# Performance work log

Hardware: AMD Instinct MI355X
Metric: run time of the kernel (lower is better)

The kernel has to match this reference:

```python
import jax, jax.numpy as jnp
import numpy as np

N_GRAPHS = 256
N_NODES = 100000
N_EDGES = 1000000
EMB = 64
EMB_RBF = 16
NUM_HEADS = 1


def setup_inputs() -> dict:
    key = jax.random.key(0)
    ks = jax.random.split(key, 10)
    edge_emb = jax.random.normal(ks[0], (N_EDGES, EMB), dtype=jnp.float32)
    edge_index = jax.random.randint(ks[1], (2, N_EDGES), 0, N_NODES, dtype=jnp.int64)
    distance_vec = jax.random.normal(ks[2], (N_EDGES, 3), dtype=jnp.float32)
    lattice = jax.random.normal(ks[3], (N_GRAPHS, 3, 3), dtype=jnp.float32)
    batch = jnp.sort(jax.random.randint(ks[4], (N_NODES,), 0, N_GRAPHS, dtype=jnp.int64))
    rbf = jax.random.uniform(ks[5], (N_EDGES, EMB_RBF), dtype=jnp.float32)
    # Dense layers (GemNet Dense defaults to bias=False)
    s = 1.0 / np.sqrt(EMB)
    W1 = jax.random.normal(ks[6], (EMB, EMB), dtype=jnp.float32) * s
    W2 = jax.random.normal(ks[7], (EMB, EMB), dtype=jnp.float32) * s
    W_rbf = jax.random.normal(ks[8], (EMB_RBF, EMB), dtype=jnp.float32) * (1.0 / np.sqrt(EMB_RBF))
    W_out = jax.random.normal(ks[9], (EMB, NUM_HEADS), dtype=jnp.float32) * s
    return {"edge_emb": edge_emb, "edge_index": edge_index, "distance_vec": distance_vec,
            "lattice": lattice, "batch": batch, "rbf": rbf,
            "W1": W1, "W2": W2, "W_rbf": W_rbf, "W_out": W_out}


def reference(edge_emb, edge_index, distance_vec, lattice, batch, rbf, W1, W2, W_rbf, W_out):
    # compute_score_per_edge: MLP on edge embeddings, gated by RBF projection
    h = jax.nn.silu(edge_emb @ W1)            # [E, EMB]
    x_F = h @ W2                               # [E, EMB]
    x_F = x_F * (rbf @ W_rbf)                  # RBF gate, [E, EMB]
    edge_scores = x_F @ W_out                  # [E, num_heads]

    batch_edge = batch[edge_index[0]]          # graph id per edge, [E]
    # normalize_score=True: divide by edge count per graph
    num_edges = jax.ops.segment_sum(jnp.ones((edge_scores.shape[0],), dtype=edge_scores.dtype),
                                    batch_edge, num_segments=N_GRAPHS)
    edge_scores = edge_scores / num_edges[batch_edge, None]

    # edge_score_to_lattice_score_frac_symmetric, summed over heads (num_heads=1)
    s = edge_scores[:, 0]                      # [E]
    unit = distance_vec / jnp.linalg.norm(distance_vec, axis=-1, keepdims=True)
    outer = s[:, None, None] * unit[:, :, None] * distance_vec[:, None, :]  # [E,3,3]
    sym = 0.5 * (outer + jnp.swapaxes(outer, 1, 2))
    out = jax.ops.segment_sum(sym, batch_edge, num_segments=N_GRAPHS)       # [B,3,3]
    return out
```

## Files before the change

### kernel.cpp

```cpp
#include <hip/hip_runtime.h>
#include <math.h>

constexpr int G    = 256;
constexpr int EMB  = 64;
constexpr int ERBF = 16;

typedef __attribute__((ext_vector_type(8))) short bf16x8;
typedef __attribute__((ext_vector_type(4))) float f32x4;

static __device__ __forceinline__ short bf16_rne(float f) {
    union { float f; unsigned u; } v; v.f = f;
    unsigned r = (v.u + 0x7FFFu + ((v.u >> 16) & 1u)) >> 16;
    return (short)r;
}

__global__ void prep_M_kernel(const float* __restrict__ W2,
                              const float* __restrict__ W_rbf,
                              const float* __restrict__ W_out,
                              float* __restrict__ M) {
    int t = blockIdx.x * blockDim.x + threadIdx.x;
    if (t >= EMB * ERBF) return;
    int p = t >> 4;
    int k = t & 15;
    float acc = 0.f;
    for (int j = 0; j < EMB; ++j)
        acc = fmaf(W2[p * EMB + j] * W_out[j], W_rbf[k * EMB + j], acc);
    M[p * ERBF + k] = acc;
}

__global__ __launch_bounds__(256, 4) void edge_kernel(
    const float* __restrict__ edge_emb,
    const int*   __restrict__ edge_src,
    const float* __restrict__ dvec,
    const int*   __restrict__ batch,
    const float* __restrict__ rbf,
    const float* __restrict__ W1,
    const float* __restrict__ M,
    float* __restrict__ partial,
    int ne, int nblk)
{
    __shared__ float accs[G * 9];

    const int tid  = threadIdx.x;
    const int w    = tid >> 6;
    const int lane = tid & 63;
    const int q    = lane >> 4;
    const int col  = lane & 15;

    for (int i = tid; i < G * 9; i += 256) accs[i] = 0.f;

    bf16x8 w1f[4][2];
#pragma unroll
    for (int nt = 0; nt < 4; ++nt)
#pragma unroll
        for (int c = 0; c < 2; ++c) {
            bf16x8 wv;
#pragma unroll
            for (int j = 0; j < 8; ++j)
                wv[j] = bf16_rne(W1[(c * 32 + q * 8 + j) * EMB + nt * 16 + col]);
            w1f[nt][c] = wv;
        }
    bf16x8 mtf[4];
#pragma unroll
    for (int nt = 0; nt < 4; ++nt) {
        bf16x8 mv;
#pragma unroll
        for (int j = 0; j < 8; ++j) {
            int k = q * 8 + j;
            mv[j] = (k < ERBF) ? bf16_rne(M[(nt * 16 + col) * ERBF + k]) : (short)0;
        }
        mtf[nt] = mv;
    }
    __syncthreads();

    const long estep = (long)nblk * 4 * 16;
    for (long e0 = ((long)blockIdx.x * 4 + w) * 16; e0 < ne; e0 += estep) {
        const long erow  = e0 + col;
        const bool rowok = (erow < ne);

        bf16x8 af[2];
#pragma unroll
        for (int c = 0; c < 2; ++c) {
            bf16x8 a;
            if (rowok) {
                const float4* p = (const float4*)(edge_emb + (size_t)erow * EMB + c * 32 + q * 8);
                float4 v0 = p[0], v1 = p[1];
                a[0] = bf16_rne(v0.x); a[1] = bf16_rne(v0.y);
                a[2] = bf16_rne(v0.z); a[3] = bf16_rne(v0.w);
                a[4] = bf16_rne(v1.x); a[5] = bf16_rne(v1.y);
                a[6] = bf16_rne(v1.z); a[7] = bf16_rne(v1.w);
            } else {
#pragma unroll
                for (int j = 0; j < 8; ++j) a[j] = 0;
            }
            af[c] = a;
        }
        bf16x8 rf;
        if (q < 2 && rowok) {
            const float4* p = (const float4*)(rbf + (size_t)erow * ERBF + q * 8);
            float4 v0 = p[0], v1 = p[1];
            rf[0] = bf16_rne(v0.x); rf[1] = bf16_rne(v0.y);
            rf[2] = bf16_rne(v0.z); rf[3] = bf16_rne(v0.w);
            rf[4] = bf16_rne(v1.x); rf[5] = bf16_rne(v1.y);
            rf[6] = bf16_rne(v1.z); rf[7] = bf16_rne(v1.w);
        } else {
#pragma unroll
            for (int j = 0; j < 8; ++j) rf[j] = 0;
        }

        f32x4 hacc[4], vacc[4];
#pragma unroll
        for (int nt = 0; nt < 4; ++nt) {
            f32x4 z = {0.f, 0.f, 0.f, 0.f};
            z = __builtin_amdgcn_mfma_f32_16x16x32_bf16(af[0], w1f[nt][0], z, 0, 0, 0);
            z = __builtin_amdgcn_mfma_f32_16x16x32_bf16(af[1], w1f[nt][1], z, 0, 0, 0);
            hacc[nt] = z;
            f32x4 zv = {0.f, 0.f, 0.f, 0.f};
            vacc[nt] = __builtin_amdgcn_mfma_f32_16x16x32_bf16(rf, mtf[nt], zv, 0, 0, 0);
        }

        float sc[4];
#pragma unroll
        for (int r = 0; r < 4; ++r) {
            float acc = 0.f;
#pragma unroll
            for (int nt = 0; nt < 4; ++nt) {
                float x = hacc[nt][r];
                float s = x * __builtin_amdgcn_rcpf(1.f + __expf(-x));
                acc = fmaf(s, vacc[nt][r], acc);
            }
            sc[r] = acc;
        }
#pragma unroll
        for (int m = 1; m < 16; m <<= 1) {
#pragma unroll
            for (int r = 0; r < 4; ++r) sc[r] += __shfl_xor(sc[r], m);
        }

        if (col < 4) {
            long e = e0 + q * 4 + col;
            if (e < ne) {
                float s = sc[col];
                int   g = batch[edge_src[e]];
                size_t de = (size_t)e * 3;
                float dx = dvec[de], dy = dvec[de + 1], dz = dvec[de + 2];
                float nrm = sqrtf(dx * dx + dy * dy + dz * dz);
                float cc = s / nrm;
                float* a = &accs[g * 9];
                atomicAdd(a + 0, cc * dx * dx);
                atomicAdd(a + 1, cc * dx * dy);
                atomicAdd(a + 2, cc * dx * dz);
                atomicAdd(a + 3, cc * dy * dy);
                atomicAdd(a + 4, cc * dy * dz);
                atomicAdd(a + 5, cc * dz * dz);
                atomicAdd(a + 6, 1.0f);
            }
        }
    }

    __syncthreads();
    float* outp = partial + (size_t)blockIdx.x * (G * 8);
    {
        int g = tid;
        float* a = &accs[g * 9];
        float4 p0 = {a[0], a[1], a[2], a[3]};
        float4 p1 = {a[4], a[5], a[6], 0.f};
        ((float4*)(outp + g * 8))[0] = p0;
        ((float4*)(outp + g * 8))[1] = p1;
    }
}

__global__ __launch_bounds__(256) void reduce_kernel(
    const float* __restrict__ partial, float* __restrict__ out, int nblk)
{
    int g = blockIdx.x;
    __shared__ float red[256][8];
    float loc[8];
#pragma unroll
    for (int c = 0; c < 8; ++c) loc[c] = 0.f;

    for (int b = threadIdx.x; b < nblk; b += 256) {
        const float4* p = (const float4*)(partial + (size_t)b * (G * 8) + g * 8);
        float4 v0 = p[0], v1 = p[1];
        loc[0] += v0.x; loc[1] += v0.y; loc[2] += v0.z; loc[3] += v0.w;
        loc[4] += v1.x; loc[5] += v1.y; loc[6] += v1.z; loc[7] += v1.w;
    }
#pragma unroll
    for (int c = 0; c < 8; ++c) red[threadIdx.x][c] = loc[c];
    __syncthreads();

    for (int off = 128; off >= 1; off >>= 1) {
        if (threadIdx.x < off) {
#pragma unroll
            for (int c = 0; c < 8; ++c)
                red[threadIdx.x][c] += red[threadIdx.x + off][c];
        }
        __syncthreads();
    }

    if (threadIdx.x == 0) {
        float cnt = red[0][6];
        float inv = (cnt > 0.f) ? (1.f / cnt) : 0.f;
        float xx = red[0][0] * inv, xy = red[0][1] * inv, xz = red[0][2] * inv;
        float yy = red[0][3] * inv, yz = red[0][4] * inv, zz = red[0][5] * inv;
        float* o = out + g * 9;
        o[0] = xx; o[1] = xy; o[2] = xz;
        o[3] = xy; o[4] = yy; o[5] = yz;
        o[6] = xz; o[7] = yz; o[8] = zz;
    }
}

extern "C" void kernel_launch(void* const* d_in, const int* in_sizes, int n_in,
                              void* d_out, int out_size, void* d_ws, size_t ws_size,
                              hipStream_t stream) {
    const float* edge_emb   = (const float*)d_in[0];
    const int*   edge_index = (const int*)  d_in[1];
    const float* dvec       = (const float*)d_in[2];
    const int*   batch      = (const int*)  d_in[4];
    const float* rbf        = (const float*)d_in[5];
    const float* W1         = (const float*)d_in[6];
    const float* W2         = (const float*)d_in[7];
    const float* W_rbf      = (const float*)d_in[8];
    const float* W_out      = (const float*)d_in[9];
    float* out = (float*)d_out;

    int ne = in_sizes[0] / EMB;

    float* M = (float*)d_ws;
    float* partial = (float*)((char*)d_ws + 4096);
    size_t avail = (ws_size > 4096) ? (ws_size - 4096) : 0;
    int nblk = (int)(avail / (G * 8 * sizeof(float)));
    int tiles = (ne + 63) / 64;
    if (nblk > 1024)  nblk = 1024;
    if (nblk > tiles) nblk = tiles;
    if (nblk < 1)     nblk = 1;

    prep_M_kernel<<<4, 256, 0, stream>>>(W2, W_rbf, W_out, M);
    edge_kernel<<<nblk, 256, 0, stream>>>(edge_emb, edge_index, dvec, batch,
                                          rbf, W1, M, partial, ne, nblk);
    reduce_kernel<<<G, 256, 0, stream>>>(partial, out, nblk);
}
```

Measured before the change: 426.9 us.

## Fuse M precompute into edge kernel, hoist gathers, transpose partial layout

Removes the separate prep_M kernel launch: each block recomputes the fused W2·W_out·W_rbf matrix into shared memory. The main loop issues the edge_src, dvec and batch gathers at the top of each iteration, before the MFMA work, and clamps out-of-range rows instead of branching, so the global loads overlap the math. The partial-sum buffer is transposed to be graph-major so the reduce kernel reads contiguously. The grid is capped at 768 blocks with launch bounds of 3 waves per SIMD. The cost is redundant per-block M computation and an extra barrier.

Result: no change. 432.8 us (+1.4%).

```diff
diff --git a/kernel.cpp b/kernel.cpp
--- a/kernel.cpp
+++ b/kernel.cpp
@@ -14,32 +14,21 @@
     return (short)r;
 }
 
-__global__ void prep_M_kernel(const float* __restrict__ W2,
-                              const float* __restrict__ W_rbf,
-                              const float* __restrict__ W_out,
-                              float* __restrict__ M) {
-    int t = blockIdx.x * blockDim.x + threadIdx.x;
-    if (t >= EMB * ERBF) return;
-    int p = t >> 4;
-    int k = t & 15;
-    float acc = 0.f;
-    for (int j = 0; j < EMB; ++j)
-        acc = fmaf(W2[p * EMB + j] * W_out[j], W_rbf[k * EMB + j], acc);
-    M[p * ERBF + k] = acc;
-}
-
-__global__ __launch_bounds__(256, 4) void edge_kernel(
+__global__ __launch_bounds__(256, 3) void edge_kernel(
     const float* __restrict__ edge_emb,
     const int*   __restrict__ edge_src,
     const float* __restrict__ dvec,
     const int*   __restrict__ batch,
     const float* __restrict__ rbf,
     const float* __restrict__ W1,
-    const float* __restrict__ M,
+    const float* __restrict__ W2,
+    const float* __restrict__ W_rbf,
+    const float* __restrict__ W_out,
     float* __restrict__ partial,
     int ne, int nblk)
 {
     __shared__ float accs[G * 9];
+    __shared__ float Msh[EMB * ERBF];
 
     const int tid  = threadIdx.x;
     const int w    = tid >> 6;
@@ -49,6 +38,23 @@
 
     for (int i = tid; i < G * 9; i += 256) accs[i] = 0.f;
 
+    {
+        int idx0 = tid * 4;
+        int p  = idx0 >> 4;
+        int k0 = idx0 & 15;
+        float m0 = 0.f, m1 = 0.f, m2 = 0.f, m3 = 0.f;
+        for (int j = 0; j < EMB; ++j) {
+            float wj = W2[p * EMB + j] * W_out[j];
+            m0 = fmaf(wj, W_rbf[(k0 + 0) * EMB + j], m0);
+            m1 = fmaf(wj, W_rbf[(k0 + 1) * EMB + j], m1);
+            m2 = fmaf(wj, W_rbf[(k0 + 2) * EMB + j], m2);
+            m3 = fmaf(wj, W_rbf[(k0 + 3) * EMB + j], m3);
+        }
+        Msh[idx0 + 0] = m0; Msh[idx0 + 1] = m1;
+        Msh[idx0 + 2] = m2; Msh[idx0 + 3] = m3;
+    }
+    __syncthreads();
+
     bf16x8 w1f[4][2];
 #pragma unroll
     for (int nt = 0; nt < 4; ++nt)
@@ -67,53 +73,63 @@
 #pragma unroll
         for (int j = 0; j < 8; ++j) {
             int k = q * 8 + j;
-            mv[j] = (k < ERBF) ? bf16_rne(M[(nt * 16 + col) * ERBF + k]) : (short)0;
+            mv[j] = (k < ERBF) ? bf16_rne(Msh[(nt * 16 + col) * ERBF + k]) : (short)0;
         }
         mtf[nt] = mv;
     }
-    __syncthreads();
 
     const long estep = (long)nblk * 4 * 16;
     for (long e0 = ((long)blockIdx.x * 4 + w) * 16; e0 < ne; e0 += estep) {
-        const long erow  = e0 + col;
-        const bool rowok = (erow < ne);
-
-        bf16x8 af[2];
-#pragma unroll
-        for (int c = 0; c < 2; ++c) {
-            bf16x8 a;
-            if (rowok) {
-                const float4* p = (const float4*)(edge_emb + (size_t)erow * EMB + c * 32 + q * 8);
-                float4 v0 = p[0], v1 = p[1];
-                a[0] = bf16_rne(v0.x); a[1] = bf16_rne(v0.y);
-                a[2] = bf16_rne(v0.z); a[3] = bf16_rne(v0.w);
-                a[4] = bf16_rne(v1.x); a[5] = bf16_rne(v1.y);
-                a[6] = bf16_rne(v1.z); a[7] = bf16_rne(v1.w);
-            } else {
-#pragma unroll
-                for (int j = 0; j < 8; ++j) a[j] = 0;
-            }
-            af[c] = a;
-        }
-        bf16x8 rf;
-        if (q < 2 && rowok) {
-            const float4* p = (const float4*)(rbf + (size_t)erow * ERBF + q * 8);
-            float4 v0 = p[0], v1 = p[1];
-            rf[0] = bf16_rne(v0.x); rf[1] = bf16_rne(v0.y);
-            rf[2] = bf16_rne(v0.z); rf[3] = bf16_rne(v0.w);
-            rf[4] = bf16_rne(v1.x); rf[5] = bf16_rne(v1.y);
-            rf[6] = bf16_rne(v1.z); rf[7] = bf16_rne(v1.w);
-        } else {
-#pragma unroll
-            for (int j = 0; j < 8; ++j) rf[j] = 0;
-        }
+        const long erow = e0 + col;
+        const long erc  = (erow < ne) ? erow : (long)(ne - 1);
+
+        const long esc = e0 + q * 4 + col;
+        const bool sok = (col < 4) && (esc < ne);
+        int src = 0; float dx = 0.f, dy = 0.f, dz = 0.f;
+        if (col < 4) {
+            long ec = (esc < ne) ? esc : (long)(ne - 1);
+            src = edge_src[ec];
+            size_t de = (size_t)ec * 3;
+            dx = dvec[de]; dy = dvec[de + 1]; dz = dvec[de + 2];
+        }
+
+        const float* rowe = edge_emb + (size_t)erc * EMB + q * 8;
+        float4 a00 = ((const float4*)rowe)[0];
+        float4 a01 = ((const float4*)rowe)[1];
+        float4 a10 = ((const float4*)(rowe + 32))[0];
+        float4 a11 = ((const float4*)(rowe + 32))[1];
+        const float4* rowr = (const float4*)(rbf + (size_t)erc * ERBF + (q & 1) * 8);
+        float4 r0 = rowr[0];
+        float4 r1 = rowr[1];
+
+        int gidx = 0;
+        if (col < 4) gidx = batch[src];
+
+        bf16x8 af0, af1, rf;
+        af0[0] = bf16_rne(a00.x); af0[1] = bf16_rne(a00.y);
+        af0[2] = bf16_rne(a00.z); af0[3] = bf16_rne(a00.w);
+        af0[4] = bf16_rne(a01.x); af0[5] = bf16_rne(a01.y);
+        af0[6] = bf16_rne(a01.z); af0[7] = bf16_rne(a01.w);
+        af1[0] = bf16_rne(a10.x); af1[1] = bf16_rne(a10.y);
+        af1[2] = bf16_rne(a10.z); af1[3] = bf16_rne(a10.w);
+        af1[4] = bf16_rne(a11.x); af1[5] = bf16_rne(a11.y);
+        af1[6] = bf16_rne(a11.z); af1[7] = bf16_rne(a11.w);
+        const bool qv = (q < 2);
+        rf[0] = qv ? bf16_rne(r0.x) : (short)0;
+        rf[1] = qv ? bf16_rne(r0.y) : (short)0;
+        rf[2] = qv ? bf16_rne(r0.z) : (short)0;
+        rf[3] = qv ? bf16_rne(r0.w) : (short)0;
+        rf[4] = qv ? bf16_rne(r1.x) : (short)0;
+        rf[5] = qv ? bf16_rne(r1.y) : (short)0;
+        rf[6] = qv ? bf16_rne(r1.z) : (short)0;
+        rf[7] = qv ? bf16_rne(r1.w) : (short)0;
 
         f32x4 hacc[4], vacc[4];
 #pragma unroll
         for (int nt = 0; nt < 4; ++nt) {
             f32x4 z = {0.f, 0.f, 0.f, 0.f};
-            z = __builtin_amdgcn_mfma_f32_16x16x32_bf16(af[0], w1f[nt][0], z, 0, 0, 0);
-            z = __builtin_amdgcn_mfma_f32_16x16x32_bf16(af[1], w1f[nt][1], z, 0, 0, 0);
+            z = __builtin_amdgcn_mfma_f32_16x16x32_bf16(af0, w1f[nt][0], z, 0, 0, 0);
+            z = __builtin_amdgcn_mfma_f32_16x16x32_bf16(af1, w1f[nt][1], z, 0, 0, 0);
             hacc[nt] = z;
             f32x4 zv = {0.f, 0.f, 0.f, 0.f};
             vacc[nt] = __builtin_amdgcn_mfma_f32_16x16x32_bf16(rf, mtf[nt], zv, 0, 0, 0);
@@ -137,36 +153,30 @@
             for (int r = 0; r < 4; ++r) sc[r] += __shfl_xor(sc[r], m);
         }
 
-        if (col < 4) {
-            long e = e0 + q * 4 + col;
-            if (e < ne) {
-                float s = sc[col];
-                int   g = batch[edge_src[e]];
-                size_t de = (size_t)e * 3;
-                float dx = dvec[de], dy = dvec[de + 1], dz = dvec[de + 2];
-                float nrm = sqrtf(dx * dx + dy * dy + dz * dz);
-                float cc = s / nrm;
-                float* a = &accs[g * 9];
-                atomicAdd(a + 0, cc * dx * dx);
-                atomicAdd(a + 1, cc * dx * dy);
-                atomicAdd(a + 2, cc * dx * dz);
-                atomicAdd(a + 3, cc * dy * dy);
-                atomicAdd(a + 4, cc * dy * dz);
-                atomicAdd(a + 5, cc * dz * dz);
-                atomicAdd(a + 6, 1.0f);
-            }
+        if (sok) {
+            float s = sc[col];
+            float nrm = sqrtf(dx * dx + dy * dy + dz * dz);
+            float cc = s / nrm;
+            float* a = &accs[gidx * 9];
+            atomicAdd(a + 0, cc * dx * dx);
+            atomicAdd(a + 1, cc * dx * dy);
+            atomicAdd(a + 2, cc * dx * dz);
+            atomicAdd(a + 3, cc * dy * dy);
+            atomicAdd(a + 4, cc * dy * dz);
+            atomicAdd(a + 5, cc * dz * dz);
+            atomicAdd(a + 6, 1.0f);
         }
     }
 
     __syncthreads();
-    float* outp = partial + (size_t)blockIdx.x * (G * 8);
     {
         int g = tid;
         float* a = &accs[g * 9];
         float4 p0 = {a[0], a[1], a[2], a[3]};
         float4 p1 = {a[4], a[5], a[6], 0.f};
-        ((float4*)(outp + g * 8))[0] = p0;
-        ((float4*)(outp + g * 8))[1] = p1;
+        float* outp = partial + (size_t)g * ((size_t)nblk * 8) + (size_t)blockIdx.x * 8;
+        ((float4*)outp)[0] = p0;
+        ((float4*)outp)[1] = p1;
     }
 }
 
@@ -179,8 +189,9 @@
 #pragma unroll
     for (int c = 0; c < 8; ++c) loc[c] = 0.f;
 
+    const float* base = partial + (size_t)g * ((size_t)nblk * 8);
     for (int b = threadIdx.x; b < nblk; b += 256) {
-        const float4* p = (const float4*)(partial + (size_t)b * (G * 8) + g * 8);
+        const float4* p = (const float4*)(base + (size_t)b * 8);
         float4 v0 = p[0], v1 = p[1];
         loc[0] += v0.x; loc[1] += v0.y; loc[2] += v0.z; loc[3] += v0.w;
         loc[4] += v1.x; loc[5] += v1.y; loc[6] += v1.z; loc[7] += v1.w;
@@ -226,17 +237,15 @@
 
     int ne = in_sizes[0] / EMB;
 
-    float* M = (float*)d_ws;
-    float* partial = (float*)((char*)d_ws + 4096);
-    size_t avail = (ws_size > 4096) ? (ws_size - 4096) : 0;
-    int nblk = (int)(avail / (G * 8 * sizeof(float)));
+    float* partial = (float*)d_ws;
+    int nblk = (int)(ws_size / (G * 8 * sizeof(float)));
     int tiles = (ne + 63) / 64;
-    if (nblk > 1024)  nblk = 1024;
+    if (nblk > 768)   nblk = 768;
     if (nblk > tiles) nblk = tiles;
     if (nblk < 1)     nblk = 1;
 
-    prep_M_kernel<<<4, 256, 0, stream>>>(W2, W_rbf, W_out, M);
     edge_kernel<<<nblk, 256, 0, stream>>>(edge_emb, edge_index, dvec, batch,
-                                          rbf, W1, M, partial, ne, nblk);
+                                          rbf, W1, W2, W_rbf, W_out,
+                                          partial, ne, nblk);
     reduce_kernel<<<G, 256, 0, stream>>>(partial, out, nblk);
 }
```
